# Performance work log

Measured on AMD Instinct MI355X. Metric: run time of the kernel, lower is better.

## Reference

```python
import jax, jax.numpy as jnp
import numpy as np
from jax import lax

N = 4096
D = 256          # dim_hidden
DU = 1024        # dim_uni
G = 2000         # num_genes
E = 4            # num_experts
K = 1            # top-k
H = 4            # attention heads
HD = D // H      # head dim = 64
MAP = 64         # fourier mapping_size


def _ln(x, g, b, eps=1e-5):
    m = jnp.mean(x, axis=-1, keepdims=True)
    v = jnp.var(x, axis=-1, keepdims=True)
    return (x - m) * lax.rsqrt(v + eps) * g + b


def setup_inputs() -> dict:
    key = jax.random.key(0)
    ks = jax.random.split(key, 32)
    s = 0.02
    inp = {
        "vis": jax.random.normal(ks[0], (N, DU), jnp.float32),
        "pos": jax.random.uniform(ks[1], (N, 3), jnp.float32),
        "grad": jax.random.uniform(ks[2], (N, 1), jnp.float32),
        # FourierEncoding buffer: randn(3, 64) * scale(10)
        "B_fourier": jax.random.normal(ks[3], (3, MAP), jnp.float32) * 10.0,
        # img_enc
        "W_img": jax.random.normal(ks[4], (DU, D), jnp.float32) * s,
        "b_img": jnp.zeros((D,), jnp.float32),
        # pos_enc linear: Linear(128, 256)
        "W_pos": jax.random.normal(ks[5], (2 * MAP, D), jnp.float32) * s,
        "b_pos": jnp.zeros((D,), jnp.float32),
        # MultiheadAttention projections
        "Wq": jax.random.normal(ks[6], (D, D), jnp.float32) * s,
        "bq": jnp.zeros((D,), jnp.float32),
        "Wk": jax.random.normal(ks[7], (D, D), jnp.float32) * s,
        "bk": jnp.zeros((D,), jnp.float32),
        "Wv": jax.random.normal(ks[8], (D, D), jnp.float32) * s,
        "bv": jnp.zeros((D,), jnp.float32),
        "Wo": jax.random.normal(ks[9], (D, D), jnp.float32) * s,
        "bo": jnp.zeros((D,), jnp.float32),
        "ln1_g": jnp.ones((D,), jnp.float32),
        "ln1_b": jnp.zeros((D,), jnp.float32),
        # MoE router: Linear(D+1, E)
        "W_router": jax.random.normal(ks[10], (D + 1, E), jnp.float32) * s,
        "b_router": jnp.zeros((E,), jnp.float32),
        # experts: stacked [E, ...] FFN weights
        "W1e": jax.random.normal(ks[11], (E, D, 4 * D), jnp.float32) * s,
        "b1e": jnp.zeros((E, 4 * D), jnp.float32),
        "W2e": jax.random.normal(ks[12], (E, 4 * D, D), jnp.float32) * s,
        "b2e": jnp.zeros((E, D), jnp.float32),
        # gene decoder
        "Wg1": jax.random.normal(ks[13], (D, D), jnp.float32) * s,
        "bg1": jnp.zeros((D,), jnp.float32),
        "lng_g": jnp.ones((D,), jnp.float32),
        "lng_b": jnp.zeros((D,), jnp.float32),
        "Wg2": jax.random.normal(ks[14], (D, 2 * G), jnp.float32) * s,
        "bg2": jnp.zeros((2 * G,), jnp.float32),
        # func head
        "Wf1": jax.random.normal(ks[15], (D, 64), jnp.float32) * s,
        "bf1": jnp.zeros((64,), jnp.float32),
        "Wf2": jax.random.normal(ks[16], (64, 1), jnp.float32) * s,
        "bf2": jnp.zeros((1,), jnp.float32),
    }
    return inp


def reference(vis, pos, grad, B_fourier, W_img, b_img, W_pos, b_pos,
              Wq, bq, Wk, bk, Wv, bv, Wo, bo, ln1_g, ln1_b,
              W_router, b_router, W1e, b1e, W2e, b2e,
              Wg1, bg1, lng_g, lng_b, Wg2, bg2, Wf1, bf1, Wf2, bf2):
    # --- encoders ---
    x_proj = (2.0 * np.pi) * (pos @ B_fourier)                 # [N, 64]
    fourier = jnp.concatenate([jnp.sin(x_proj), jnp.cos(x_proj)], axis=-1)  # [N,128]
    z = vis @ W_img + b_img + fourier @ W_pos + b_pos          # [N, D]

    # --- spatial context attention (batch=1 full self-attention) ---
    q = (z @ Wq + bq).reshape(N, H, HD)
    k = (z @ Wk + bk).reshape(N, H, HD)
    v = (z @ Wv + bv).reshape(N, H, HD)
    scores = jnp.einsum('nhd,mhd->hnm', q, k) / np.sqrt(HD)    # [H, N, N]
    attn = jax.nn.softmax(scores, axis=-1)
    ctx = jnp.einsum('hnm,mhd->nhd', attn, v).reshape(N, D)
    attn_out = ctx @ Wo + bo
    z = _ln(z + attn_out, ln1_g, ln1_b)

    # --- sparse MoE (top-1 routing, gated dense expert combine) ---
    router_in = jnp.concatenate([z, grad], axis=-1)            # [N, D+1]
    logits = router_in @ W_router + b_router                   # [N, E]
    probs = jax.nn.softmax(logits, axis=-1)
    topk_p, topk_i = lax.top_k(probs, K)                       # [N, K]
    gate = jnp.sum(jax.nn.one_hot(topk_i, E, dtype=z.dtype) * topk_p[..., None], axis=1)  # [N, E]
    h = jax.nn.gelu(jnp.einsum('nd,edf->nef', z, W1e) + b1e, approximate=False)  # [N,E,4D]
    y = jnp.einsum('nef,efd->ned', h, W2e) + b2e               # [N, E, D]
    z = z + jnp.einsum('ne,ned->nd', gate, y)

    # --- gene decoder ---
    d = jax.nn.gelu(_ln(z @ Wg1 + bg1, lng_g, lng_b), approximate=False)
    preds = (d @ Wg2 + bg2).reshape(N, G, 2)
    mu = jax.nn.softplus(preds[:, :, 0])
    theta = jax.nn.softplus(preds[:, :, 1]) + 1e-6

    # --- functional head ---
    g = jax.nn.sigmoid(jax.nn.gelu(z @ Wf1 + bf1, approximate=False) @ Wf2 + bf2)
    return mu, theta, g
```

## Files before the change

kernel.cpp:

```cpp
#include <hip/hip_runtime.h>
#include <math.h>

#define NTOK 4096
#define DMODEL 256
#define G_GENES 2000

typedef _Float16 f16;
typedef _Float16 f16x8 __attribute__((ext_vector_type(8)));
typedef float f32x4 __attribute__((ext_vector_type(4)));

__device__ __forceinline__ float gelu_exact(float x) {
    return 0.5f * x * (1.0f + erff(x * 0.70710678118654752f));
}
__device__ __forceinline__ float softplus_fast(float x) {
    return fmaxf(x, 0.0f) + __logf(1.0f + __expf(-fabsf(x)));
}

__global__ __launch_bounds__(64) void fourier_k(const float* __restrict__ pos,
                                                const float* __restrict__ B,
                                                f16* __restrict__ Abig) {
    int n = blockIdx.x, m = threadIdx.x;
    float xp = 6.283185307179586f *
               (pos[n * 3 + 0] * B[m] + pos[n * 3 + 1] * B[64 + m] + pos[n * 3 + 2] * B[128 + m]);
    Abig[(size_t)n * 1152 + 1024 + m] = (f16)sinf(xp);
    Abig[(size_t)n * 1152 + 1088 + m] = (f16)cosf(xp);
}

__global__ __launch_bounds__(256) void cvt_vis_k(const float* __restrict__ vis, f16* __restrict__ Abig) {
    int n = blockIdx.x, t = threadIdx.x;
    float4 v = *(const float4*)(vis + (size_t)n * 1024 + t * 4);
    union { ushort4 u; f16 h[4]; } o;
    o.h[0] = (f16)v.x; o.h[1] = (f16)v.y; o.h[2] = (f16)v.z; o.h[3] = (f16)v.w;
    *(ushort4*)(Abig + (size_t)n * 1152 + t * 4) = o.u;
}

struct TD { const float* s; f16* d; int R, C; int ldo; };
struct TDs { TD t[17]; int pre[18]; };
__global__ __launch_bounds__(256) void tconv_k(TDs ds) {
    int bid = blockIdx.x;
    int ti = 0;
#pragma unroll
    for (int i = 0; i < 17; i++)
        if (bid >= ds.pre[i + 1]) ti = i + 1;
    TD td = ds.t[ti];
    int local = bid - ds.pre[ti];
    int yt = td.C >> 5;
    int r0 = (local / yt) << 5;
    int c0 = (local % yt) << 5;
    __shared__ float tile[32][33];
    int tx = threadIdx.x & 31, ty = threadIdx.x >> 5;
#pragma unroll
    for (int i = 0; i < 32; i += 8)
        tile[ty + i][tx] = td.s[(size_t)(r0 + ty + i) * td.C + c0 + tx];
    __syncthreads();
#pragma unroll
    for (int i = 0; i < 32; i += 8)
        td.d[(size_t)(c0 + ty + i) * td.ldo + r0 + tx] = (f16)tile[tx][ty + i];
}

__global__ __launch_bounds__(256) void tconvh_k(const f16* __restrict__ src, int ldin,
                                                f16* __restrict__ dst, int ldo) {
    __shared__ f16 tile[32][33];
    int r0 = blockIdx.x * 32, c0 = blockIdx.y * 32;
    int tx = threadIdx.x & 31, ty = threadIdx.x >> 5;
#pragma unroll
    for (int i = 0; i < 32; i += 8)
        tile[ty + i][tx] = src[(size_t)(r0 + ty + i) * ldin + c0 + tx];
    __syncthreads();
#pragma unroll
    for (int i = 0; i < 32; i += 8)
        dst[(size_t)(c0 + ty + i) * ldo + r0 + tx] = tile[tx][ty + i];
}

__global__ __launch_bounds__(256) void addbias_k(const float* a, const float* b, float* o) {
    int t = threadIdx.x;
    o[t] = a[t] + b[t];
}

#define EPI_F32 0
#define EPI_DUAL 1
#define EPI_F16 2
#define EPI_GELU_F16 3
#define EPI_GENE 4
#define EPI_MOESC 5

template <int MTN, int EPI, int MODE>
__global__ __launch_bounds__(256) void bgemm_k(
    const f16* __restrict__ A, int lda,
    const f16* __restrict__ B, int ldb,
    const float* __restrict__ bias,
    float* __restrict__ Cf, f16* __restrict__ Ch, int ldc,
    int Ncols, int K,
    size_t eB, size_t eBias,
    const int* __restrict__ gidx, const int* __restrict__ temap,
    const float* __restrict__ z2, const float* __restrict__ gval,
    float* __restrict__ outMu, float* __restrict__ outTheta) {
    constexpr int BN = MTN * 32;
    __shared__ __align__(16) char smem[(128 + BN) * 72 * 2];
    f16 (*As)[72] = (f16(*)[72])smem;
    f16 (*Bs)[72] = (f16(*)[72])(smem + (size_t)128 * 72 * 2);

    const int tid = threadIdx.x;
    const int m0 = blockIdx.x * 128;
    const int n0 = blockIdx.y * BN;
    const int w = tid >> 6, lane = tid & 63;
    const int wr = w >> 1, wc = w & 1;
    const int ln = lane & 15, lg = lane >> 4;
    const int sr = tid >> 3;
    const int sc = (tid & 7) * 8;

    if (MODE == 1 || MODE == 2) {
        int e = temap[blockIdx.x];
        B += (size_t)e * eB;
        if (bias) bias += (size_t)e * eBias;
    }

    int grows[4];
#pragma unroll
    for (int i = 0; i < 4; i++) {
        int r = m0 + sr + i * 32;
        if (MODE == 1) {
            int g = gidx[r];
            grows[i] = (g < 0) ? 0 : g;
        } else {
            grows[i] = r;
        }
    }

    f32x4 acc[4][MTN];
    f32x4 zf = {0.f, 0.f, 0.f, 0.f};
#pragma unroll
    for (int i = 0; i < 4; i++)
#pragma unroll
        for (int j = 0; j < MTN; j++) acc[i][j] = zf;

    for (int k0 = 0; k0 < K; k0 += 64) {
#pragma unroll
        for (int i = 0; i < 4; i++) {
            uint4 v = *(const uint4*)(A + (size_t)grows[i] * lda + k0 + sc);
            int r = sr + i * 32;
            *(uint2*)&As[r][sc] = make_uint2(v.x, v.y);
            *(uint2*)&As[r][sc + 4] = make_uint2(v.z, v.w);
        }
#pragma unroll
        for (int i = 0; i < MTN; i++) {
            int r = sr + i * 32;
            uint4 v = make_uint4(0, 0, 0, 0);
            if (n0 + r < Ncols) v = *(const uint4*)(B + (size_t)(n0 + r) * ldb + k0 + sc);
            *(uint2*)&Bs[r][sc] = make_uint2(v.x, v.y);
            *(uint2*)&Bs[r][sc + 4] = make_uint2(v.z, v.w);
        }
        __syncthreads();
#pragma unroll
        for (int ks = 0; ks < 64; ks += 32) {
            f16x8 a[4], b[MTN];
#pragma unroll
            for (int t = 0; t < 4; t++) {
                const f16* p = &As[wr * 64 + t * 16 + ln][ks + lg * 8];
                union { f16x8 f; uint2 u[2]; } tmp;
                tmp.u[0] = *(const uint2*)p;
                tmp.u[1] = *(const uint2*)(p + 4);
                a[t] = tmp.f;
            }
#pragma unroll
            for (int t = 0; t < MTN; t++) {
                const f16* p = &Bs[wc * (MTN * 16) + t * 16 + ln][ks + lg * 8];
                union { f16x8 f; uint2 u[2]; } tmp;
                tmp.u[0] = *(const uint2*)p;
                tmp.u[1] = *(const uint2*)(p + 4);
                b[t] = tmp.f;
            }
#pragma unroll
            for (int tm = 0; tm < 4; tm++)
#pragma unroll
                for (int tn = 0; tn < MTN; tn++)
                    acc[tm][tn] = __builtin_amdgcn_mfma_f32_16x16x32_f16(a[tm], b[tn], acc[tm][tn], 0, 0, 0);
        }
        __syncthreads();
    }

    if (EPI == EPI_GENE) {
        float bval[MTN];
#pragma unroll
        for (int tn = 0; tn < MTN; tn++) {
            int col = n0 + wc * (MTN * 16) + tn * 16 + ln;
            bval[tn] = (col < Ncols) ? bias[col] : 0.0f;
        }
        float* Cs = (float*)smem;
        const int rrow = tid >> 3;
        const int rseg = tid & 7;
#pragma unroll
        for (int tm = 0; tm < 4; tm++) {
            __syncthreads();
#pragma unroll
            for (int tn = 0; tn < MTN; tn++) {
                int lc = wc * (MTN * 16) + tn * 16 + ln;
#pragma unroll
                for (int i = 0; i < 4; i++) {
                    int lr = wr * 16 + lg * 4 + i;
                    Cs[lr * 132 + lc] = acc[tm][tn][i] + bval[tn];
                }
            }
            __syncthreads();
            int grow = m0 + ((rrow >> 4) * 64) + tm * 16 + (rrow & 15);
            const float* cr = &Cs[rrow * 132 + rseg * 16];
            float mu[8], th[8];
#pragma unroll
            for (int g = 0; g < 8; g++) {
                mu[g] = softplus_fast(cr[2 * g]);
                th[g] = softplus_fast(cr[2 * g + 1]) + 1e-6f;
            }
            int gbase = (n0 + rseg * 16) >> 1;
            float* mp = outMu + (size_t)grow * G_GENES + gbase;
            float* tp = outTheta + (size_t)grow * G_GENES + gbase;
            if (gbase + 8 <= G_GENES) {
                *(float4*)mp = make_float4(mu[0], mu[1], mu[2], mu[3]);
                *(float4*)(mp + 4) = make_float4(mu[4], mu[5], mu[6], mu[7]);
                *(float4*)tp = make_float4(th[0], th[1], th[2], th[3]);
                *(float4*)(tp + 4) = make_float4(th[4], th[5], th[6], th[7]);
            } else {
#pragma unroll
                for (int g = 0; g < 8; g++)
                    if (gbase + g < G_GENES) { mp[g] = mu[g]; tp[g] = th[g]; }
            }
        }
        return;
    }

#pragma unroll
    for (int tm = 0; tm < 4; tm++) {
#pragma unroll
        for (int tn = 0; tn < MTN; tn++) {
            int col = n0 + wc * (MTN * 16) + tn * 16 + ln;
            if (col >= Ncols) continue;
#pragma unroll
            for (int i = 0; i < 4; i++) {
                int row = m0 + wr * 64 + tm * 16 + lg * 4 + i;
                float v = acc[tm][tn][i];
                if (EPI == EPI_MOESC) {
                    int tok = gidx[row];
                    if (tok < 0) continue;
                    v += bias[col];
                    size_t oi = (size_t)tok * ldc + col;
                    Ch[oi] = (f16)(z2[oi] + gval[tok] * v);
                    continue;
                }
                size_t idx = (size_t)row * ldc + col;
                if (EPI == EPI_F32) {
                    if (bias) v += bias[col];
                    Cf[idx] = v;
                } else if (EPI == EPI_DUAL) {
                    v += bias[col];
                    Cf[idx] = v;
                    Ch[idx] = (f16)v;
                } else if (EPI == EPI_F16) {
                    v += bias[col];
                    Ch[idx] = (f16)v;
                } else if (EPI == EPI_GELU_F16) {
                    v += bias[col];
                    Ch[idx] = (f16)gelu_exact(v);
                }
            }
        }
    }
}

__global__ __launch_bounds__(256) void flash_k(const f16* __restrict__ qkv,
                                               const f16* __restrict__ Vt,
                                               float* __restrict__ Opart,
                                               float2* __restrict__ mlpart) {
    __shared__ f16 Ks[64][72];
    __shared__ f16 Vts[64][72];
    __shared__ f16 Ps[4][16][72];
    const int tid = threadIdx.x;
    const int w = tid >> 6, lane = tid & 63;
    const int ln = lane & 15, quad = lane >> 4;
    const int q0 = blockIdx.x * 64;
    const int hq = blockIdx.y * 64;
    const int kt0 = blockIdx.z * 16;

    f16x8 qfrag[2];
    {
        const f16* qp = qkv + (size_t)(q0 + w * 16 + ln) * 768 + hq + quad * 8;
        union { f16x8 f; uint4 u; } t0, t1;
        t0.u = *(const uint4*)qp;
        t1.u = *(const uint4*)(qp + 32);
        qfrag[0] = t0.f; qfrag[1] = t1.f;
    }

    const int srow = tid >> 2;
    const int scol = (tid & 3) * 16;

    float m_run[4], l_run[4];
    f32x4 Oacc[4];
#pragma unroll
    for (int i = 0; i < 4; i++) {
        m_run[i] = -1e30f; l_run[i] = 0.0f;
        Oacc[i] = (f32x4){0.f, 0.f, 0.f, 0.f};
    }

    uint4 kreg[2], vreg[2];
    {
        const f16* kp = qkv + (size_t)(kt0 * 64 + srow) * 768 + 256 + hq + scol;
        const f16* vp = Vt + (size_t)(hq + srow) * 4096 + kt0 * 64 + scol;
        kreg[0] = *(const uint4*)kp; kreg[1] = *(const uint4*)(kp + 8);
        vreg[0] = *(const uint4*)vp; vreg[1] = *(const uint4*)(vp + 8);
    }

    for (int kt = kt0; kt < kt0 + 16; kt++) {
        __syncthreads();
        *(uint4*)&Ks[srow][scol] = kreg[0];
        *(uint4*)&Ks[srow][scol + 8] = kreg[1];
        *(uint4*)&Vts[srow][scol] = vreg[0];
        *(uint4*)&Vts[srow][scol + 8] = vreg[1];
        __syncthreads();
        if (kt + 1 < kt0 + 16) {
            const f16* kp = qkv + (size_t)((kt + 1) * 64 + srow) * 768 + 256 + hq + scol;
            const f16* vp = Vt + (size_t)(hq + srow) * 4096 + (kt + 1) * 64 + scol;
            kreg[0] = *(const uint4*)kp; kreg[1] = *(const uint4*)(kp + 8);
            vreg[0] = *(const uint4*)vp; vreg[1] = *(const uint4*)(vp + 8);
        }

        f32x4 accS[4];
#pragma unroll
        for (int nt = 0; nt < 4; nt++) {
            union { f16x8 f; uint4 u; } b0, b1;
            b0.u = *(const uint4*)&Ks[nt * 16 + ln][quad * 8];
            b1.u = *(const uint4*)&Ks[nt * 16 + ln][32 + quad * 8];
            f32x4 a = {0.f, 0.f, 0.f, 0.f};
            a = __builtin_amdgcn_mfma_f32_16x16x32_f16(qfrag[0], b0.f, a, 0, 0, 0);
            a = __builtin_amdgcn_mfma_f32_16x16x32_f16(qfrag[1], b1.f, a, 0, 0, 0);
            accS[nt] = a;
        }
#pragma unroll
        for (int nt = 0; nt < 4; nt++)
#pragma unroll
            for (int i = 0; i < 4; i++) accS[nt][i] *= 0.125f;

        float mnew[4], alpha[4], rs[4];
#pragma unroll
        for (int i = 0; i < 4; i++) {
            float mx = fmaxf(fmaxf(accS[0][i], accS[1][i]), fmaxf(accS[2][i], accS[3][i]));
            mx = fmaxf(mx, __shfl_xor(mx, 1));
            mx = fmaxf(mx, __shfl_xor(mx, 2));
            mx = fmaxf(mx, __shfl_xor(mx, 4));
            mx = fmaxf(mx, __shfl_xor(mx, 8));
            mnew[i] = fmaxf(m_run[i], mx);
            rs[i] = 0.0f;
        }
#pragma unroll
        for (int nt = 0; nt < 4; nt++)
#pragma unroll
            for (int i = 0; i < 4; i++) {
                float p = __expf(accS[nt][i] - mnew[i]);
                accS[nt][i] = p;
                rs[i] += p;
            }
#pragma unroll
        for (int i = 0; i < 4; i++) {
            float s = rs[i];
            s += __shfl_xor(s, 1);
            s += __shfl_xor(s, 2);
            s += __shfl_xor(s, 4);
            s += __shfl_xor(s, 8);
            alpha[i] = __expf(m_run[i] - mnew[i]);
            l_run[i] = l_run[i] * alpha[i] + s;
            m_run[i] = mnew[i];
        }
#pragma unroll
        for (int dt = 0; dt < 4; dt++)
#pragma unroll
            for (int i = 0; i < 4; i++) Oacc[dt][i] *= alpha[i];

#pragma unroll
        for (int nt = 0; nt < 4; nt++)
#pragma unroll
            for (int i = 0; i < 4; i++)
                Ps[w][quad * 4 + i][nt * 16 + ln] = (f16)accS[nt][i];

        union { f16x8 f; uint4 u; } pf0, pf1;
        pf0.u = *(const uint4*)&Ps[w][ln][quad * 8];
        pf1.u = *(const uint4*)&Ps[w][ln][32 + quad * 8];
#pragma unroll
        for (int dt = 0; dt < 4; dt++) {
            union { f16x8 f; uint4 u; } b0, b1;
            b0.u = *(const uint4*)&Vts[dt * 16 + ln][quad * 8];
            b1.u = *(const uint4*)&Vts[dt * 16 + ln][32 + quad * 8];
            Oacc[dt] = __builtin_amdgcn_mfma_f32_16x16x32_f16(pf0.f, b0.f, Oacc[dt], 0, 0, 0);
            Oacc[dt] = __builtin_amdgcn_mfma_f32_16x16x32_f16(pf1.f, b1.f, Oacc[dt], 0, 0, 0);
        }
    }

    const int s = blockIdx.z;
#pragma unroll
    for (int dt = 0; dt < 4; dt++)
#pragma unroll
        for (int i = 0; i < 4; i++)
            Opart[((size_t)(s * NTOK) + q0 + w * 16 + quad * 4 + i) * 256 + hq + dt * 16 + ln] =
                Oacc[dt][i];
    if (ln == 0) {
#pragma unroll
        for (int i = 0; i < 4; i++)
            mlpart[(size_t)(s * 4 + blockIdx.y) * NTOK + q0 + w * 16 + quad * 4 + i] =
                make_float2(m_run[i], l_run[i]);
    }
}

__global__ __launch_bounds__(256) void fcomb_k(const float* __restrict__ Opart,
                                               const float2* __restrict__ mlpart,
                                               f16* __restrict__ ctxbf) {
    int t = blockIdx.x * 256 + threadIdx.x;
    int n = t >> 6;
    int rem = t & 63;
    int h = rem >> 4;
    int d4 = (rem & 15) * 4;
    float2 ml[4];
    float mmax = -1e30f;
#pragma unroll
    for (int s = 0; s < 4; s++) {
        ml[s] = mlpart[(size_t)(s * 4 + h) * NTOK + n];
        mmax = fmaxf(mmax, ml[s].x);
    }
    float wgt[4], l = 0.0f;
#pragma unroll
    for (int s = 0; s < 4; s++) {
        wgt[s] = __expf(ml[s].x - mmax);
        l += wgt[s] * ml[s].y;
    }
    float4 o = {0.f, 0.f, 0.f, 0.f};
#pragma unroll
    for (int s = 0; s < 4; s++) {
        float4 p = *(const float4*)(Opart + ((size_t)(s * NTOK) + n) * 256 + h * 64 + d4);
        o.x += wgt[s] * p.x; o.y += wgt[s] * p.y;
        o.z += wgt[s] * p.z; o.w += wgt[s] * p.w;
    }
    float inv = 1.0f / l;
    union { ushort4 u; f16 hh[4]; } pk;
    pk.hh[0] = (f16)(o.x * inv); pk.hh[1] = (f16)(o.y * inv);
    pk.hh[2] = (f16)(o.z * inv); pk.hh[3] = (f16)(o.w * inv);
    *(ushort4*)(ctxbf + (size_t)n * 256 + h * 64 + d4) = pk.u;
}

__global__ __launch_bounds__(256) void ln_k(const float* __restrict__ X,
                                            const float* __restrict__ R,
                                            const float* __restrict__ gam,
                                            const float* __restrict__ bet,
                                            float* __restrict__ Of, f16* __restrict__ Oh, int doGelu) {
    __shared__ float sm[4];
    int n = blockIdx.x, c = threadIdx.x;
    float x = X[(size_t)n * DMODEL + c];
    if (R) x += R[(size_t)n * DMODEL + c];
    float s = x;
    for (int off = 32; off; off >>= 1) s += __shfl_down(s, off);
    if ((c & 63) == 0) sm[c >> 6] = s;
    __syncthreads();
    float mean = (sm[0] + sm[1] + sm[2] + sm[3]) * (1.0f / DMODEL);
    float d = x - mean;
    float s2 = d * d;
    for (int off = 32; off; off >>= 1) s2 += __shfl_down(s2, off);
    __syncthreads();
    if ((c & 63) == 0) sm[c >> 6] = s2;
    __syncthreads();
    float var = (sm[0] + sm[1] + sm[2] + sm[3]) * (1.0f / DMODEL);
    float y = d * rsqrtf(var + 1e-5f) * gam[c] + bet[c];
    if (doGelu) y = gelu_exact(y);
    size_t idx = (size_t)n * DMODEL + c;
    if (Of) Of[idx] = y;
    if (Oh) Oh[idx] = (f16)y;
}

__global__ __launch_bounds__(64) void router_k(const float* __restrict__ z2,
                                               const float* __restrict__ grad,
                                               const float* __restrict__ Wr,
                                               const float* __restrict__ br,
                                               int* __restrict__ eid,
                                               float* __restrict__ gval) {
    int n = blockIdx.x, t = threadIdx.x;
    float p0 = 0, p1 = 0, p2 = 0, p3 = 0;
#pragma unroll
    for (int i = 0; i < 4; i++) {
        int d = t + i * 64;
        float zv = z2[(size_t)n * DMODEL + d];
        p0 = fmaf(zv, Wr[d * 4 + 0], p0);
        p1 = fmaf(zv, Wr[d * 4 + 1], p1);
        p2 = fmaf(zv, Wr[d * 4 + 2], p2);
        p3 = fmaf(zv, Wr[d * 4 + 3], p3);
    }
    for (int off = 32; off; off >>= 1) {
        p0 += __shfl_down(p0, off);
        p1 += __shfl_down(p1, off);
        p2 += __shfl_down(p2, off);
        p3 += __shfl_down(p3, off);
    }
    if (t == 0) {
        float gv = grad[n];
        float l[4];
        l[0] = p0 + gv * Wr[256 * 4 + 0] + br[0];
        l[1] = p1 + gv * Wr[256 * 4 + 1] + br[1];
        l[2] = p2 + gv * Wr[256 * 4 + 2] + br[2];
        l[3] = p3 + gv * Wr[256 * 4 + 3] + br[3];
        float mx = fmaxf(fmaxf(l[0], l[1]), fmaxf(l[2], l[3]));
        float e[4], s = 0;
#pragma unroll
        for (int i = 0; i < 4; i++) { e[i] = __expf(l[i] - mx); s += e[i]; }
        int am = 0;
        float best = l[0];
#pragma unroll
        for (int i = 1; i < 4; i++)
            if (l[i] > best) { best = l[i]; am = i; }
        eid[n] = am;
        gval[n] = e[am] / s;
    }
}

__global__ __launch_bounds__(256) void compact_k(const int* __restrict__ eid,
                                                 int* __restrict__ gidx,
                                                 int* __restrict__ temap) {
    __shared__ int cnt[4], poff[4], cur[4];
    int t = threadIdx.x;
    if (t < 4) cnt[t] = 0;
    __syncthreads();
    for (int it = 0; it < 16; it++)
        atomicAdd(&cnt[eid[it * 256 + t]], 1);
    __syncthreads();
    if (t == 0) {
        int o = 0;
        for (int e = 0; e < 4; e++) {
            poff[e] = o;
            cur[e] = o;
            o += (cnt[e] + 127) & ~127;
        }
    }
    __syncthreads();
    if (t < 36) {
        int e = 0;
        for (int x = 0; x < 4; x++) {
            int seg0 = poff[x] >> 7;
            int seg1 = (poff[x] + ((cnt[x] + 127) & ~127)) >> 7;
            if (t >= seg0 && t < seg1) e = x;
        }
        temap[t] = e;
    }
    for (int i = t; i < 4608; i += 256) gidx[i] = -1;
    __syncthreads();
    for (int it = 0; it < 16; it++) {
        int n = it * 256 + t;
        int slot = atomicAdd(&cur[eid[n]], 1);
        gidx[slot] = n;
    }
}

__global__ __launch_bounds__(256) void ghead_k(const f16* __restrict__ f,
                                               const float* __restrict__ Wf2,
                                               const float* __restrict__ bf2,
                                               float* __restrict__ out) {
    int n = blockIdx.x * 256 + threadIdx.x;
    float s = bf2[0];
#pragma unroll
    for (int c = 0; c < 8; c++) {
        union { uint4 u; f16 h[8]; } t;
        t.u = *(const uint4*)(f + (size_t)n * 64 + c * 8);
#pragma unroll
        for (int j = 0; j < 8; j++) s = fmaf((float)t.h[j], Wf2[c * 8 + j], s);
    }
    out[n] = 1.0f / (1.0f + expf(-s));
}

extern "C" void kernel_launch(void* const* d_in, const int* in_sizes, int n_in,
                              void* d_out, int out_size, void* d_ws, size_t ws_size,
                              hipStream_t stream) {
    const float* vis   = (const float*)d_in[0];
    const float* pos   = (const float*)d_in[1];
    const float* grad  = (const float*)d_in[2];
    const float* Bf    = (const float*)d_in[3];
    const float* W_img = (const float*)d_in[4];
    const float* b_img = (const float*)d_in[5];
    const float* W_pos = (const float*)d_in[6];
    const float* b_pos = (const float*)d_in[7];
    const float* Wq = (const float*)d_in[8];  const float* bq = (const float*)d_in[9];
    const float* Wk = (const float*)d_in[10]; const float* bk = (const float*)d_in[11];
    const float* Wv = (const float*)d_in[12]; const float* bv = (const float*)d_in[13];
    const float* Wo = (const float*)d_in[14]; const float* bo = (const float*)d_in[15];
    const float* ln1g = (const float*)d_in[16]; const float* ln1b = (const float*)d_in[17];
    const float* Wr = (const float*)d_in[18]; const float* br = (const float*)d_in[19];
    const float* W1e = (const float*)d_in[20]; const float* b1e = (const float*)d_in[21];
    const float* W2e = (const float*)d_in[22]; const float* b2e = (const float*)d_in[23];
    const float* Wg1 = (const float*)d_in[24]; const float* bg1 = (const float*)d_in[25];
    const float* lngg = (const float*)d_in[26]; const float* lngb = (const float*)d_in[27];
    const float* Wg2 = (const float*)d_in[28]; const float* bg2 = (const float*)d_in[29];
    const float* Wf1 = (const float*)d_in[30]; const float* bf1 = (const float*)d_in[31];
    const float* Wf2 = (const float*)d_in[32]; const float* bf2 = (const float*)d_in[33];

    float* out = (float*)d_out;
    float* outMu = out;
    float* outTh = out + (size_t)NTOK * G_GENES;
    float* outG  = out + (size_t)2 * NTOK * G_GENES;

    char* base = (char*)d_ws;
    size_t off = 0;
    auto A8 = [&](size_t bytes) { char* p = base + off; off += (bytes + 255) & ~(size_t)255; return p; };

    char* reg1 = A8(16 * 1024 * 1024);
    f16*   Abig  = (f16*)reg1;
    float* Opart = (float*)reg1;
    char* reg2 = A8(20 * 1024 * 1024);
    f16* qkvbf = (f16*)reg2;
    f16* hh    = (f16*)(reg2 + 8 * 1024 * 1024);

    f16* WtEnc = (f16*)A8((size_t)256 * 1152 * 2);
    f16* Wqkvt = (f16*)A8((size_t)768 * 256 * 2);
    f16* Wot   = (f16*)A8((size_t)256 * 256 * 2);
    f16* W1t   = (f16*)A8((size_t)4 * 1024 * 256 * 2);
    f16* W2t   = (f16*)A8((size_t)4 * 256 * 1024 * 2);
    f16* Wg1t  = (f16*)A8((size_t)256 * 256 * 2);
    f16* Wg2t  = (f16*)A8((size_t)4000 * 256 * 2);
    f16* Wf1t  = (f16*)A8((size_t)64 * 256 * 2);
    f16* Vt    = (f16*)A8((size_t)256 * NTOK * 2);
    float2* mlpart = (float2*)A8((size_t)16 * NTOK * 8);
    float* benc    = (float*)A8(256 * 4);
    float* biasqkv = (float*)A8(768 * 4);
    float* z    = (float*)A8((size_t)NTOK * DMODEL * 4);
    float* z2   = (float*)A8((size_t)NTOK * DMODEL * 4);
    float* attn = (float*)A8((size_t)NTOK * DMODEL * 4);
    float* tbuf = (float*)A8((size_t)NTOK * DMODEL * 4);
    f16* zbf    = (f16*)A8((size_t)NTOK * DMODEL * 2);
    f16* z2bf   = (f16*)A8((size_t)NTOK * DMODEL * 2);
    f16* z3bf   = (f16*)A8((size_t)NTOK * DMODEL * 2);
    f16* ctxbf  = (f16*)A8((size_t)NTOK * DMODEL * 2);
    f16* dbufbf = (f16*)A8((size_t)NTOK * DMODEL * 2);
    f16* fbf    = (f16*)A8((size_t)NTOK * 64 * 2);
    int* eidb   = (int*)A8(NTOK * 4);
    float* gval = (float*)A8(NTOK * 4);
    int* gidx   = (int*)A8(4608 * 4);
    int* temap  = (int*)A8(64 * 4);

    dim3 blk(256);

    TDs td;
    int nd = 0, pre = 0;
    auto addT = [&](const float* s, f16* d, int R, int C, int ldo) {
        td.t[nd] = TD{s, d, R, C, ldo};
        td.pre[nd] = pre;
        pre += (R >> 5) * (C >> 5);
        nd++;
    };
    addT(W_img, WtEnc, 1024, 256, 1152);
    addT(W_pos, WtEnc + 1024, 128, 256, 1152);
    addT(Wq, Wqkvt, 256, 256, 256);
    addT(Wk, Wqkvt + 256 * 256, 256, 256, 256);
    addT(Wv, Wqkvt + 512 * 256, 256, 256, 256);
    addT(Wo, Wot, 256, 256, 256);
    for (int e = 0; e < 4; e++) addT(W1e + (size_t)e * 262144, W1t + (size_t)e * 262144, 256, 1024, 256);
    for (int e = 0; e < 4; e++) addT(W2e + (size_t)e * 262144, W2t + (size_t)e * 262144, 1024, 256, 1024);
    addT(Wg1, Wg1t, 256, 256, 256);
    addT(Wg2, Wg2t, 256, 4000, 256);
    addT(Wf1, Wf1t, 256, 64, 256);
    td.pre[nd] = pre;
    tconv_k<<<pre, blk, 0, stream>>>(td);
    addbias_k<<<1, blk, 0, stream>>>(b_img, b_pos, benc);
    hipMemcpyAsync(biasqkv, bq, 256 * 4, hipMemcpyDeviceToDevice, stream);
    hipMemcpyAsync(biasqkv + 256, bk, 256 * 4, hipMemcpyDeviceToDevice, stream);
    hipMemcpyAsync(biasqkv + 512, bv, 256 * 4, hipMemcpyDeviceToDevice, stream);

    cvt_vis_k<<<NTOK, blk, 0, stream>>>(vis, Abig);
    fourier_k<<<NTOK, 64, 0, stream>>>(pos, Bf, Abig);
    bgemm_k<1, EPI_DUAL, 0><<<dim3(32, 8, 1), blk, 0, stream>>>(
        Abig, 1152, WtEnc, 1152, benc, z, zbf, 256, 256, 1152,
        0, 0, nullptr, nullptr, nullptr, nullptr, nullptr, nullptr);

    bgemm_k<2, EPI_F16, 0><<<dim3(32, 12, 1), blk, 0, stream>>>(
        zbf, 256, Wqkvt, 256, biasqkv, nullptr, qkvbf, 768, 768, 256,
        0, 0, nullptr, nullptr, nullptr, nullptr, nullptr, nullptr);
    tconvh_k<<<dim3(128, 8, 1), blk, 0, stream>>>(qkvbf + 512, 768, Vt, 4096);

    flash_k<<<dim3(64, 4, 4), blk, 0, stream>>>(qkvbf, Vt, Opart, mlpart);
    fcomb_k<<<1024, blk, 0, stream>>>(Opart, mlpart, ctxbf);
    bgemm_k<1, EPI_F32, 0><<<dim3(32, 8, 1), blk, 0, stream>>>(
        ctxbf, 256, Wot, 256, bo, attn, nullptr, 256, 256, 256,
        0, 0, nullptr, nullptr, nullptr, nullptr, nullptr, nullptr);
    ln_k<<<NTOK, blk, 0, stream>>>(z, attn, ln1g, ln1b, z2, z2bf, 0);

    router_k<<<NTOK, 64, 0, stream>>>(z2, grad, Wr, br, eidb, gval);
    compact_k<<<1, blk, 0, stream>>>(eidb, gidx, temap);
    bgemm_k<4, EPI_GELU_F16, 1><<<dim3(36, 8, 1), blk, 0, stream>>>(
        z2bf, 256, W1t, 256, b1e, nullptr, hh, 1024, 1024, 256,
        262144, 1024, gidx, temap, nullptr, nullptr, nullptr, nullptr);
    bgemm_k<2, EPI_MOESC, 2><<<dim3(36, 4, 1), blk, 0, stream>>>(
        hh, 1024, W2t, 1024, b2e, nullptr, z3bf, 256, 256, 1024,
        262144, 256, gidx, temap, z2, gval, nullptr, nullptr);

    bgemm_k<1, EPI_F32, 0><<<dim3(32, 8, 1), blk, 0, stream>>>(
        z3bf, 256, Wg1t, 256, bg1, tbuf, nullptr, 256, 256, 256,
        0, 0, nullptr, nullptr, nullptr, nullptr, nullptr, nullptr);
    ln_k<<<NTOK, blk, 0, stream>>>(tbuf, nullptr, lngg, lngb, nullptr, dbufbf, 1);
    bgemm_k<4, EPI_GENE, 0><<<dim3(32, 32, 1), blk, 0, stream>>>(
        dbufbf, 256, Wg2t, 256, bg2, nullptr, nullptr, 4000, 4000, 256,
        0, 0, nullptr, nullptr, nullptr, nullptr, outMu, outTh);

    bgemm_k<1, EPI_GELU_F16, 0><<<dim3(32, 2, 1), blk, 0, stream>>>(
        z3bf, 256, Wf1t, 256, bf1, nullptr, fbf, 64, 64, 256,
        0, 0, nullptr, nullptr, nullptr, nullptr, nullptr, nullptr);
    ghead_k<<<NTOK / 256, blk, 0, stream>>>(fbf, Wf2, bf2, outG);
}
```

Before: 454.9 us.

## Fuse small kernels, split flash KV 8 ways with fp16 partials, merge decoder GEMMs

Merges the vis-convert and Fourier kernels, the bias-setup kernel and its memcpys, and the router into the LayerNorm kernel. The Wg1 and Wf1 GEMMs now run as one 320-column GEMM with a split epilogue. Flash attention splits the KV range 8 ways instead of 4 and stores partial outputs in fp16 in a fragment-native layout, so the combine kernel reads them contiguously. The aim is fewer launches, more parallelism in attention and less partial-output traffic, at the cost of some precision in the partial sums.

```diff
diff --git a/kernel.cpp b/kernel.cpp
--- a/kernel.cpp
+++ b/kernel.cpp
@@ -16,22 +16,21 @@
     return fmaxf(x, 0.0f) + __logf(1.0f + __expf(-fabsf(x)));
 }
 
-__global__ __launch_bounds__(64) void fourier_k(const float* __restrict__ pos,
-                                                const float* __restrict__ B,
-                                                f16* __restrict__ Abig) {
-    int n = blockIdx.x, m = threadIdx.x;
-    float xp = 6.283185307179586f *
-               (pos[n * 3 + 0] * B[m] + pos[n * 3 + 1] * B[64 + m] + pos[n * 3 + 2] * B[128 + m]);
-    Abig[(size_t)n * 1152 + 1024 + m] = (f16)sinf(xp);
-    Abig[(size_t)n * 1152 + 1088 + m] = (f16)cosf(xp);
-}
-
-__global__ __launch_bounds__(256) void cvt_vis_k(const float* __restrict__ vis, f16* __restrict__ Abig) {
+__global__ __launch_bounds__(256) void encin_k(const float* __restrict__ vis,
+                                               const float* __restrict__ pos,
+                                               const float* __restrict__ B,
+                                               f16* __restrict__ Abig) {
     int n = blockIdx.x, t = threadIdx.x;
     float4 v = *(const float4*)(vis + (size_t)n * 1024 + t * 4);
     union { ushort4 u; f16 h[4]; } o;
     o.h[0] = (f16)v.x; o.h[1] = (f16)v.y; o.h[2] = (f16)v.z; o.h[3] = (f16)v.w;
     *(ushort4*)(Abig + (size_t)n * 1152 + t * 4) = o.u;
+    if (t < 64) {
+        float xp = 6.283185307179586f *
+                   (pos[n * 3 + 0] * B[t] + pos[n * 3 + 1] * B[64 + t] + pos[n * 3 + 2] * B[128 + t]);
+        Abig[(size_t)n * 1152 + 1024 + t] = (f16)sinf(xp);
+        Abig[(size_t)n * 1152 + 1088 + t] = (f16)cosf(xp);
+    }
 }
 
 struct TD { const float* s; f16* d; int R, C; int ldo; };
@@ -72,9 +71,17 @@
         dst[(size_t)(c0 + ty + i) * ldo + r0 + tx] = tile[tx][ty + i];
 }
 
-__global__ __launch_bounds__(256) void addbias_k(const float* a, const float* b, float* o) {
+__global__ __launch_bounds__(256) void setup_k(const float* b_img, const float* b_pos,
+                                               const float* bq, const float* bk, const float* bv,
+                                               const float* bg1, const float* bf1,
+                                               float* benc, float* biasqkv, float* bgf) {
     int t = threadIdx.x;
-    o[t] = a[t] + b[t];
+    benc[t] = b_img[t] + b_pos[t];
+    biasqkv[t] = bq[t];
+    biasqkv[256 + t] = bk[t];
+    biasqkv[512 + t] = bv[t];
+    bgf[t] = bg1[t];
+    if (t < 64) bgf[256 + t] = bf1[t];
 }
 
 #define EPI_F32 0
@@ -83,6 +90,7 @@
 #define EPI_GELU_F16 3
 #define EPI_GENE 4
 #define EPI_MOESC 5
+#define EPI_GF 6
 
 template <int MTN, int EPI, int MODE>
 __global__ __launch_bounds__(256) void bgemm_k(
@@ -243,6 +251,12 @@
                     v += bias[col];
                     size_t oi = (size_t)tok * ldc + col;
                     Ch[oi] = (f16)(z2[oi] + gval[tok] * v);
+                    continue;
+                }
+                if (EPI == EPI_GF) {
+                    v += bias[col];
+                    if (col < 256) Cf[(size_t)row * 256 + col] = v;
+                    else Ch[(size_t)row * 64 + (col - 256)] = (f16)gelu_exact(v);
                     continue;
                 }
                 size_t idx = (size_t)row * ldc + col;
@@ -267,7 +281,7 @@
 
 __global__ __launch_bounds__(256) void flash_k(const f16* __restrict__ qkv,
                                                const f16* __restrict__ Vt,
-                                               float* __restrict__ Opart,
+                                               f16* __restrict__ Opart16,
                                                float2* __restrict__ mlpart) {
     __shared__ f16 Ks[64][72];
     __shared__ f16 Vts[64][72];
@@ -277,7 +291,7 @@
     const int ln = lane & 15, quad = lane >> 4;
     const int q0 = blockIdx.x * 64;
     const int hq = blockIdx.y * 64;
-    const int kt0 = blockIdx.z * 16;
+    const int kt0 = blockIdx.z * 8;
 
     f16x8 qfrag[2];
     {
@@ -307,14 +321,14 @@
         vreg[0] = *(const uint4*)vp; vreg[1] = *(const uint4*)(vp + 8);
     }
 
-    for (int kt = kt0; kt < kt0 + 16; kt++) {
+    for (int kt = kt0; kt < kt0 + 8; kt++) {
         __syncthreads();
         *(uint4*)&Ks[srow][scol] = kreg[0];
         *(uint4*)&Ks[srow][scol + 8] = kreg[1];
         *(uint4*)&Vts[srow][scol] = vreg[0];
         *(uint4*)&Vts[srow][scol + 8] = vreg[1];
         __syncthreads();
-        if (kt + 1 < kt0 + 16) {
+        if (kt + 1 < kt0 + 8) {
             const f16* kp = qkv + (size_t)((kt + 1) * 64 + srow) * 768 + 256 + hq + scol;
             const f16* vp = Vt + (size_t)(hq + srow) * 4096 + (kt + 1) * 64 + scol;
             kreg[0] = *(const uint4*)kp; kreg[1] = *(const uint4*)(kp + 8);
@@ -391,62 +405,95 @@
         }
     }
 
-    const int s = blockIdx.z;
-#pragma unroll
-    for (int dt = 0; dt < 4; dt++)
+    const int slot = blockIdx.x * 4 + blockIdx.y;
+    f16* op = Opart16 + ((((size_t)blockIdx.z * 256 + slot) * 4 + w) * 64 + lane) * 16;
+    union { uint4 u; f16 h[8]; } pk0, pk1;
+#pragma unroll
+    for (int dt = 0; dt < 2; dt++)
+#pragma unroll
+        for (int i = 0; i < 4; i++) pk0.h[dt * 4 + i] = (f16)Oacc[dt][i];
+#pragma unroll
+    for (int dt = 2; dt < 4; dt++)
+#pragma unroll
+        for (int i = 0; i < 4; i++) pk1.h[(dt - 2) * 4 + i] = (f16)Oacc[dt][i];
+    *(uint4*)op = pk0.u;
+    *(uint4*)(op + 8) = pk1.u;
+    if (ln == 0) {
 #pragma unroll
         for (int i = 0; i < 4; i++)
-            Opart[((size_t)(s * NTOK) + q0 + w * 16 + quad * 4 + i) * 256 + hq + dt * 16 + ln] =
-                Oacc[dt][i];
-    if (ln == 0) {
-#pragma unroll
-        for (int i = 0; i < 4; i++)
-            mlpart[(size_t)(s * 4 + blockIdx.y) * NTOK + q0 + w * 16 + quad * 4 + i] =
+            mlpart[(size_t)(blockIdx.z * 4 + blockIdx.y) * NTOK + q0 + w * 16 + quad * 4 + i] =
                 make_float2(m_run[i], l_run[i]);
     }
 }
 
-__global__ __launch_bounds__(256) void fcomb_k(const float* __restrict__ Opart,
+__global__ __launch_bounds__(256) void fcomb_k(const f16* __restrict__ Opart16,
                                                const float2* __restrict__ mlpart,
                                                f16* __restrict__ ctxbf) {
-    int t = blockIdx.x * 256 + threadIdx.x;
-    int n = t >> 6;
-    int rem = t & 63;
-    int h = rem >> 4;
-    int d4 = (rem & 15) * 4;
-    float2 ml[4];
-    float mmax = -1e30f;
-#pragma unroll
-    for (int s = 0; s < 4; s++) {
-        ml[s] = mlpart[(size_t)(s * 4 + h) * NTOK + n];
-        mmax = fmaxf(mmax, ml[s].x);
-    }
-    float wgt[4], l = 0.0f;
-#pragma unroll
-    for (int s = 0; s < 4; s++) {
-        wgt[s] = __expf(ml[s].x - mmax);
-        l += wgt[s] * ml[s].y;
-    }
-    float4 o = {0.f, 0.f, 0.f, 0.f};
-#pragma unroll
-    for (int s = 0; s < 4; s++) {
-        float4 p = *(const float4*)(Opart + ((size_t)(s * NTOK) + n) * 256 + h * 64 + d4);
-        o.x += wgt[s] * p.x; o.y += wgt[s] * p.y;
-        o.z += wgt[s] * p.z; o.w += wgt[s] * p.w;
-    }
-    float inv = 1.0f / l;
-    union { ushort4 u; f16 hh[4]; } pk;
-    pk.hh[0] = (f16)(o.x * inv); pk.hh[1] = (f16)(o.y * inv);
-    pk.hh[2] = (f16)(o.z * inv); pk.hh[3] = (f16)(o.w * inv);
-    *(ushort4*)(ctxbf + (size_t)n * 256 + h * 64 + d4) = pk.u;
-}
-
+    const int slot = blockIdx.x;
+    const int w = threadIdx.x >> 6, lane = threadIdx.x & 63;
+    const int bx = slot >> 2, h = slot & 3;
+    const int quad = lane >> 4, ln = lane & 15;
+    const int nbase = bx * 64 + w * 16 + quad * 4;
+
+    float2 ml[8][4];
+    float mmax[4] = {-1e30f, -1e30f, -1e30f, -1e30f};
+#pragma unroll
+    for (int s = 0; s < 8; s++)
+#pragma unroll
+        for (int i = 0; i < 4; i++) {
+            ml[s][i] = mlpart[(size_t)(s * 4 + h) * NTOK + nbase + i];
+            mmax[i] = fmaxf(mmax[i], ml[s][i].x);
+        }
+    float L[4] = {0.f, 0.f, 0.f, 0.f};
+    float wgt[8][4];
+#pragma unroll
+    for (int s = 0; s < 8; s++)
+#pragma unroll
+        for (int i = 0; i < 4; i++) {
+            wgt[s][i] = __expf(ml[s][i].x - mmax[i]);
+            L[i] += wgt[s][i] * ml[s][i].y;
+        }
+
+    float acc[16];
+#pragma unroll
+    for (int j = 0; j < 16; j++) acc[j] = 0.f;
+#pragma unroll
+    for (int s = 0; s < 8; s++) {
+        const f16* op = Opart16 + ((((size_t)s * 256 + slot) * 4 + w) * 64 + lane) * 16;
+        union { uint4 u; f16 h[8]; } p0, p1;
+        p0.u = *(const uint4*)op;
+        p1.u = *(const uint4*)(op + 8);
+#pragma unroll
+        for (int dt = 0; dt < 2; dt++)
+#pragma unroll
+            for (int i = 0; i < 4; i++) acc[dt * 4 + i] += wgt[s][i] * (float)p0.h[dt * 4 + i];
+#pragma unroll
+        for (int dt = 2; dt < 4; dt++)
+#pragma unroll
+            for (int i = 0; i < 4; i++) acc[dt * 4 + i] += wgt[s][i] * (float)p1.h[(dt - 2) * 4 + i];
+    }
+    float inv[4];
+#pragma unroll
+    for (int i = 0; i < 4; i++) inv[i] = 1.0f / L[i];
+#pragma unroll
+    for (int dt = 0; dt < 4; dt++)
+#pragma unroll
+        for (int i = 0; i < 4; i++)
+            ctxbf[(size_t)(nbase + i) * 256 + h * 64 + dt * 16 + ln] = (f16)(acc[dt * 4 + i] * inv[i]);
+}
+
+template <int DO_ROUTER>
 __global__ __launch_bounds__(256) void ln_k(const float* __restrict__ X,
                                             const float* __restrict__ R,
                                             const float* __restrict__ gam,
                                             const float* __restrict__ bet,
-                                            float* __restrict__ Of, f16* __restrict__ Oh, int doGelu) {
+                                            float* __restrict__ Of, f16* __restrict__ Oh, int doGelu,
+                                            const float* __restrict__ grad,
+                                            const float* __restrict__ Wr,
+                                            const float* __restrict__ br,
+                                            int* __restrict__ eid, float* __restrict__ gval) {
     __shared__ float sm[4];
+    __shared__ float smr[16];
     int n = blockIdx.x, c = threadIdx.x;
     float x = X[(size_t)n * DMODEL + c];
     if (R) x += R[(size_t)n * DMODEL + c];
@@ -467,49 +514,40 @@
     size_t idx = (size_t)n * DMODEL + c;
     if (Of) Of[idx] = y;
     if (Oh) Oh[idx] = (f16)y;
-}
-
-__global__ __launch_bounds__(64) void router_k(const float* __restrict__ z2,
-                                               const float* __restrict__ grad,
-                                               const float* __restrict__ Wr,
-                                               const float* __restrict__ br,
-                                               int* __restrict__ eid,
-                                               float* __restrict__ gval) {
-    int n = blockIdx.x, t = threadIdx.x;
-    float p0 = 0, p1 = 0, p2 = 0, p3 = 0;
-#pragma unroll
-    for (int i = 0; i < 4; i++) {
-        int d = t + i * 64;
-        float zv = z2[(size_t)n * DMODEL + d];
-        p0 = fmaf(zv, Wr[d * 4 + 0], p0);
-        p1 = fmaf(zv, Wr[d * 4 + 1], p1);
-        p2 = fmaf(zv, Wr[d * 4 + 2], p2);
-        p3 = fmaf(zv, Wr[d * 4 + 3], p3);
-    }
-    for (int off = 32; off; off >>= 1) {
-        p0 += __shfl_down(p0, off);
-        p1 += __shfl_down(p1, off);
-        p2 += __shfl_down(p2, off);
-        p3 += __shfl_down(p3, off);
-    }
-    if (t == 0) {
-        float gv = grad[n];
-        float l[4];
-        l[0] = p0 + gv * Wr[256 * 4 + 0] + br[0];
-        l[1] = p1 + gv * Wr[256 * 4 + 1] + br[1];
-        l[2] = p2 + gv * Wr[256 * 4 + 2] + br[2];
-        l[3] = p3 + gv * Wr[256 * 4 + 3] + br[3];
-        float mx = fmaxf(fmaxf(l[0], l[1]), fmaxf(l[2], l[3]));
-        float e[4], s = 0;
-#pragma unroll
-        for (int i = 0; i < 4; i++) { e[i] = __expf(l[i] - mx); s += e[i]; }
-        int am = 0;
-        float best = l[0];
-#pragma unroll
-        for (int i = 1; i < 4; i++)
-            if (l[i] > best) { best = l[i]; am = i; }
-        eid[n] = am;
-        gval[n] = e[am] / s;
+
+    if (DO_ROUTER) {
+        float p0 = y * Wr[c * 4 + 0], p1 = y * Wr[c * 4 + 1];
+        float p2 = y * Wr[c * 4 + 2], p3 = y * Wr[c * 4 + 3];
+        for (int off = 32; off; off >>= 1) {
+            p0 += __shfl_down(p0, off);
+            p1 += __shfl_down(p1, off);
+            p2 += __shfl_down(p2, off);
+            p3 += __shfl_down(p3, off);
+        }
+        int wv = c >> 6;
+        if ((c & 63) == 0) {
+            smr[wv * 4 + 0] = p0; smr[wv * 4 + 1] = p1;
+            smr[wv * 4 + 2] = p2; smr[wv * 4 + 3] = p3;
+        }
+        __syncthreads();
+        if (c == 0) {
+            float gv = grad[n];
+            float l[4];
+#pragma unroll
+            for (int e = 0; e < 4; e++)
+                l[e] = smr[e] + smr[4 + e] + smr[8 + e] + smr[12 + e] + gv * Wr[256 * 4 + e] + br[e];
+            float mx = fmaxf(fmaxf(l[0], l[1]), fmaxf(l[2], l[3]));
+            float ex[4], ssum = 0;
+#pragma unroll
+            for (int e = 0; e < 4; e++) { ex[e] = __expf(l[e] - mx); ssum += ex[e]; }
+            int am = 0;
+            float best = l[0];
+#pragma unroll
+            for (int e = 1; e < 4; e++)
+                if (l[e] > best) { best = l[e]; am = e; }
+            eid[n] = am;
+            gval[n] = ex[am] / ssum;
+        }
     }
 }
 
@@ -601,8 +639,8 @@
     auto A8 = [&](size_t bytes) { char* p = base + off; off += (bytes + 255) & ~(size_t)255; return p; };
 
     char* reg1 = A8(16 * 1024 * 1024);
-    f16*   Abig  = (f16*)reg1;
-    float* Opart = (float*)reg1;
+    f16* Abig    = (f16*)reg1;
+    f16* Opart16 = (f16*)reg1;
     char* reg2 = A8(20 * 1024 * 1024);
     f16* qkvbf = (f16*)reg2;
     f16* hh    = (f16*)(reg2 + 8 * 1024 * 1024);
@@ -612,13 +650,13 @@
     f16* Wot   = (f16*)A8((size_t)256 * 256 * 2);
     f16* W1t   = (f16*)A8((size_t)4 * 1024 * 256 * 2);
     f16* W2t   = (f16*)A8((size_t)4 * 256 * 1024 * 2);
-    f16* Wg1t  = (f16*)A8((size_t)256 * 256 * 2);
+    f16* Wgft  = (f16*)A8((size_t)320 * 256 * 2);
     f16* Wg2t  = (f16*)A8((size_t)4000 * 256 * 2);
-    f16* Wf1t  = (f16*)A8((size_t)64 * 256 * 2);
     f16* Vt    = (f16*)A8((size_t)256 * NTOK * 2);
-    float2* mlpart = (float2*)A8((size_t)16 * NTOK * 8);
+    float2* mlpart = (float2*)A8((size_t)32 * NTOK * 8);
     float* benc    = (float*)A8(256 * 4);
     float* biasqkv = (float*)A8(768 * 4);
+    float* bgf     = (float*)A8(320 * 4);
     float* z    = (float*)A8((size_t)NTOK * DMODEL * 4);
     float* z2   = (float*)A8((size_t)NTOK * DMODEL * 4);
     float* attn = (float*)A8((size_t)NTOK * DMODEL * 4);
@@ -652,18 +690,14 @@
     addT(Wo, Wot, 256, 256, 256);
     for (int e = 0; e < 4; e++) addT(W1e + (size_t)e * 262144, W1t + (size_t)e * 262144, 256, 1024, 256);
     for (int e = 0; e < 4; e++) addT(W2e + (size_t)e * 262144, W2t + (size_t)e * 262144, 1024, 256, 1024);
-    addT(Wg1, Wg1t, 256, 256, 256);
+    addT(Wg1, Wgft, 256, 256, 256);
+    addT(Wf1, Wgft + 256 * 256, 256, 64, 256);
     addT(Wg2, Wg2t, 256, 4000, 256);
-    addT(Wf1, Wf1t, 256, 64, 256);
     td.pre[nd] = pre;
     tconv_k<<<pre, blk, 0, stream>>>(td);
-    addbias_k<<<1, blk, 0, stream>>>(b_img, b_pos, benc);
-    hipMemcpyAsync(biasqkv, bq, 256 * 4, hipMemcpyDeviceToDevice, stream);
-    hipMemcpyAsync(biasqkv + 256, bk, 256 * 4, hipMemcpyDeviceToDevice, stream);
-    hipMemcpyAsync(biasqkv + 512, bv, 256 * 4, hipMemcpyDeviceToDevice, stream);
-
-    cvt_vis_k<<<NTOK, blk, 0, stream>>>(vis, Abig);
-    fourier_k<<<NTOK, 64, 0, stream>>>(pos, Bf, Abig);
+    setup_k<<<1, blk, 0, stream>>>(b_img, b_pos, bq, bk, bv, bg1, bf1, benc, biasqkv, bgf);
+
+    encin_k<<<NTOK, blk, 0, stream>>>(vis, pos, Bf, Abig);
     bgemm_k<1, EPI_DUAL, 0><<<dim3(32, 8, 1), blk, 0, stream>>>(
         Abig, 1152, WtEnc, 1152, benc, z, zbf, 256, 256, 1152,
         0, 0, nullptr, nullptr, nullptr, nullptr, nullptr, nullptr);
@@ -673,14 +707,13 @@
         0, 0, nullptr, nullptr, nullptr, nullptr, nullptr, nullptr);
     tconvh_k<<<dim3(128, 8, 1), blk, 0, stream>>>(qkvbf + 512, 768, Vt, 4096);
 
-    flash_k<<<dim3(64, 4, 4), blk, 0, stream>>>(qkvbf, Vt, Opart, mlpart);
-    fcomb_k<<<1024, blk, 0, stream>>>(Opart, mlpart, ctxbf);
+    flash_k<<<dim3(64, 4, 8), blk, 0, stream>>>(qkvbf, Vt, Opart16, mlpart);
+    fcomb_k<<<256, blk, 0, stream>>>(Opart16, mlpart, ctxbf);
     bgemm_k<1, EPI_F32, 0><<<dim3(32, 8, 1), blk, 0, stream>>>(
         ctxbf, 256, Wot, 256, bo, attn, nullptr, 256, 256, 256,
         0, 0, nullptr, nullptr, nullptr, nullptr, nullptr, nullptr);
-    ln_k<<<NTOK, blk, 0, stream>>>(z, attn, ln1g, ln1b, z2, z2bf, 0);
-
-    router_k<<<NTOK, 64, 0, stream>>>(z2, grad, Wr, br, eidb, gval);
+    ln_k<1><<<NTOK, blk, 0, stream>>>(z, attn, ln1g, ln1b, z2, z2bf, 0, grad, Wr, br, eidb, gval);
+
     compact_k<<<1, blk, 0, stream>>>(eidb, gidx, temap);
     bgemm_k<4, EPI_GELU_F16, 1><<<dim3(36, 8, 1), blk, 0, stream>>>(
         z2bf, 256, W1t, 256, b1e, nullptr, hh, 1024, 1024, 256,
@@ -689,16 +722,14 @@
         hh, 1024, W2t, 1024, b2e, nullptr, z3bf, 256, 256, 1024,
         262144, 256, gidx, temap, z2, gval, nullptr, nullptr);
 
-    bgemm_k<1, EPI_F32, 0><<<dim3(32, 8, 1), blk, 0, stream>>>(
-        z3bf, 256, Wg1t, 256, bg1, tbuf, nullptr, 256, 256, 256,
+    bgemm_k<1, EPI_GF, 0><<<dim3(32, 10, 1), blk, 0, stream>>>(
+        z3bf, 256, Wgft, 256, bgf, tbuf, fbf, 256, 320, 256,
         0, 0, nullptr, nullptr, nullptr, nullptr, nullptr, nullptr);
-    ln_k<<<NTOK, blk, 0, stream>>>(tbuf, nullptr, lngg, lngb, nullptr, dbufbf, 1);
+    ln_k<0><<<NTOK, blk, 0, stream>>>(tbuf, nullptr, lngg, lngb, nullptr, dbufbf, 1,
+                                      nullptr, nullptr, nullptr, nullptr, nullptr);
     bgemm_k<4, EPI_GENE, 0><<<dim3(32, 32, 1), blk, 0, stream>>>(
         dbufbf, 256, Wg2t, 256, bg2, nullptr, nullptr, 4000, 4000, 256,
         0, 0, nullptr, nullptr, nullptr, nullptr, outMu, outTh);
 
-    bgemm_k<1, EPI_GELU_F16, 0><<<dim3(32, 2, 1), blk, 0, stream>>>(
-        z3bf, 256, Wf1t, 256, bf1, nullptr, fbf, 64, 64, 256,
-        0, 0, nullptr, nullptr, nullptr, nullptr, nullptr, nullptr);
     ghead_k<<<NTOK / 256, blk, 0, stream>>>(fbf, Wf2, bf2, outG);
 }
```

After: 479.2 us. +5.3%, slower.
